# Kernel tuning notes

Hardware: AMD Instinct MI355X
Metric: run time of the kernel (lower is better)

Reference implementation:

```python
import jax, jax.numpy as jnp
import numpy as np

N = 50000   # nodes
E = 800000  # edges
H = 3       # attention heads
IN_F = 128
HID = 128
NUM_CLASSES = 6
GAT_SLOPE = 0.2   # DGL GATConv internal leaky_relu slope
ACT_SLOPE = 0.01  # nn.LeakyReLU default


def setup_inputs() -> dict:
    key = jax.random.key(0)
    ks = jax.random.split(key, 24)
    s = 0.05
    inp = {
        "in_feat": jax.random.normal(ks[0], (N, IN_F), jnp.float32),
        "src": jax.random.randint(ks[1], (E,), 0, N, jnp.int32),
        "dst": jax.random.randint(ks[2], (E,), 0, N, jnp.int32),
        # GATConv 1: W (IN_F, H*HID), attn vectors (H, HID), bias (H*HID)
        "W1": jax.random.normal(ks[3], (IN_F, H * HID), jnp.float32) * s,
        "al1": jax.random.normal(ks[4], (H, HID), jnp.float32) * s,
        "ar1": jax.random.normal(ks[5], (H, HID), jnp.float32) * s,
        "b1": jnp.zeros((H * HID,), jnp.float32),
        # GATConv 2
        "W2": jax.random.normal(ks[6], (HID, H * HID), jnp.float32) * s,
        "al2": jax.random.normal(ks[7], (H, HID), jnp.float32) * s,
        "ar2": jax.random.normal(ks[8], (H, HID), jnp.float32) * s,
        "b2": jnp.zeros((H * HID,), jnp.float32),
    }
    # Dense MLP head lin1..lin4 (HID->HID) and lin5 (HID->NUM_CLASSES)
    for i in range(1, 5):
        inp[f"lw{i}"] = jax.random.normal(ks[8 + 2 * i], (HID, HID), jnp.float32) * s
        inp[f"lb{i}"] = jnp.zeros((HID,), jnp.float32)
    inp["lw5"] = jax.random.normal(ks[20], (HID, NUM_CLASSES), jnp.float32) * s
    inp["lb5"] = jnp.zeros((NUM_CLASSES,), jnp.float32)
    return inp


def gat_conv(x, src, dst, W, al, ar, b):
    # x: (N, F_in) -> out: (N, H, HID)
    h = (x @ W).reshape(N, H, HID)
    el = jnp.einsum('nhf,hf->nh', h, al)  # (N, H)
    er = jnp.einsum('nhf,hf->nh', h, ar)
    e = jax.nn.leaky_relu(el[src] + er[dst], GAT_SLOPE)  # (E, H)
    # edge softmax over incoming edges of each dst node
    m = jax.ops.segment_max(e, dst, num_segments=N)
    m = jnp.where(jnp.isfinite(m), m, 0.0)
    ex = jnp.exp(e - m[dst])
    denom = jax.ops.segment_sum(ex, dst, num_segments=N)
    alpha = ex / (denom[dst] + 1e-9)  # (E, H)
    out = jax.ops.segment_sum(alpha[:, :, None] * h[src], dst, num_segments=N)
    return out + b.reshape(1, H, HID)


def reference(in_feat, src, dst, W1, al1, ar1, b1, W2, al2, ar2, b2,
              lw1, lb1, lw2, lb2, lw3, lb3, lw4, lb4, lw5, lb5):
    act = lambda x: jax.nn.leaky_relu(x, ACT_SLOPE)
    h = act(gat_conv(in_feat, src, dst, W1, al1, ar1, b1)).mean(axis=1)
    h = act(gat_conv(h, src, dst, W2, al2, ar2, b2)).mean(axis=1)
    h = act(h @ lw1 + lb1)
    h = act(h @ lw2 + lb2)
    h = act(h @ lw3 + lb3)
    h = act(h @ lw4 + lb4)
    return h @ lw5 + lb5
```

## Files before the change

### kernel.cpp

```cpp
#include <hip/hip_runtime.h>
#include <hip/hip_bf16.h>


typedef __attribute__((ext_vector_type(8))) short short8;
typedef __attribute__((ext_vector_type(4))) float float4v;

__device__ inline short f2bf(float x) {
    union { float f; unsigned u; } v; v.f = x;
    unsigned r = v.u + 0x7FFFu + ((v.u >> 16) & 1u);
    return (short)(r >> 16);
}
__device__ inline float bf2f(short b) {
    union { float f; unsigned u; } v;
    v.u = ((unsigned)(unsigned short)b) << 16;
    return v.f;
}
__device__ inline short8 zero8() { short8 z = {0,0,0,0,0,0,0,0}; return z; }

__device__ __forceinline__ void gl_lds16(const short* g, short* l) {
    __builtin_amdgcn_global_load_lds(
        (const __attribute__((address_space(1))) void*)g,
        (__attribute__((address_space(3))) void*)l,
        16, 0, 0);
}

#define SW(r) ((((r) >> 2) ^ (r)) & 3)

#define BM 128
#define BN 128
#define BK 32
#define MSTR 136
#define MROWS 64

__global__ void prep_kernel(
    const float* __restrict__ in_feat, short* __restrict__ P1h,
    int n4, int cb, int wb,
    const int* __restrict__ dst, int* __restrict__ cnt, int E,
    const float* __restrict__ w1, const float* __restrict__ w2,
    const float* __restrict__ m1, const float* __restrict__ m2,
    const float* __restrict__ m3, const float* __restrict__ m4,
    const float* __restrict__ w5,
    short* __restrict__ w1h, short* __restrict__ w2h,
    short* __restrict__ m1h, short* __restrict__ m1l,
    short* __restrict__ m2h, short* __restrict__ m2l,
    short* __restrict__ m3h, short* __restrict__ m3l,
    short* __restrict__ m4h, short* __restrict__ m4l,
    short* __restrict__ w5h, short* __restrict__ w5l,
    const float* __restrict__ al1, const float* __restrict__ ar1,
    const float* __restrict__ al2, const float* __restrict__ ar2,
    float* __restrict__ u1, float* __restrict__ u2)
{
    int blk = blockIdx.x;
    if (blk < cb) {
        int i = blk * 256 + threadIdx.x;
        if (i >= n4) return;
        float4 v = *(const float4*)(in_feat + (size_t)i * 4);
        float xs[4] = {v.x, v.y, v.z, v.w};
        short hs[4];
        #pragma unroll
        for (int j = 0; j < 4; ++j) hs[j] = f2bf(xs[j]);
        *(uint2*)(P1h + (size_t)i * 4) = *(uint2*)hs;
    } else if (blk < cb + wb) {
        int j = (blk - cb) * 256 + threadIdx.x;
        const float* src; short* th; short* tl; int Nc, base;
        if      (j < 49152)  { src = w1; th = w1h; tl = nullptr; Nc = 384; base = 0; }
        else if (j < 98304)  { src = w2; th = w2h; tl = nullptr; Nc = 384; base = 49152; }
        else if (j < 114688) { src = m1; th = m1h; tl = m1l; Nc = 128; base = 98304; }
        else if (j < 131072) { src = m2; th = m2h; tl = m2l; Nc = 128; base = 114688; }
        else if (j < 147456) { src = m3; th = m3h; tl = m3l; Nc = 128; base = 131072; }
        else if (j < 163840) { src = m4; th = m4h; tl = m4l; Nc = 128; base = 147456; }
        else if (j < 164608) { src = w5; th = w5h; tl = w5l; Nc = 6;   base = 163840; }
        else return;
        int i = j - base;
        int k = i / Nc, c = i - k * Nc;
        float v = src[i];
        short h = f2bf(v);
        th[(size_t)c * 128 + k] = h;
        if (tl) tl[(size_t)c * 128 + k] = f2bf(v - bf2f(h));
    } else if (blk == cb + wb) {
        int t = threadIdx.x;
        const float* W  = (t < 128) ? w1 : w2;
        const float* av = (t < 128) ? al1 : al2;
        const float* rv = (t < 128) ? ar1 : ar2;
        float* u = (t < 128) ? u1 : u2;
        int k = t & 127;
        #pragma unroll
        for (int h = 0; h < 3; ++h) {
            float sl = 0.f, sr = 0.f;
            for (int f = 0; f < 128; ++f) {
                float wv = W[(size_t)k * 384 + h * 128 + f];
                sl += wv * av[h * 128 + f];
                sr += wv * rv[h * 128 + f];
            }
            u[(h * 2 + 0) * 128 + k] = sl;
            u[(h * 2 + 1) * 128 + k] = sr;
        }
    } else {
        int e = (blk - cb - wb - 1) * 256 + threadIdx.x;
        if (e < E) atomicAdd(&cnt[dst[e]], 1);
    }
}

template <bool BF16>
__global__ __launch_bounds__(256) void node_el(
    const void* __restrict__ Xv, const float* __restrict__ u,
    float* __restrict__ els, float* __restrict__ er, int N)
{
    int n = blockIdx.x * 4 + (threadIdx.x >> 6);
    int l = threadIdx.x & 63;
    if (n >= N) return;
    float x0, x1;
    if (BF16) {
        unsigned v = *(const unsigned*)((const short*)Xv + (size_t)n * 128 + 2 * l);
        union { unsigned u; float f; } f0, f1;
        f0.u = v << 16; f1.u = v & 0xffff0000u;
        x0 = f0.f; x1 = f1.f;
    } else {
        float2 x = *(const float2*)((const float*)Xv + (size_t)n * 128 + 2 * l);
        x0 = x.x; x1 = x.y;
    }
    float a[6];
    #pragma unroll
    for (int v = 0; v < 6; ++v)
        a[v] = x0 * u[v * 128 + 2 * l] + x1 * u[v * 128 + 2 * l + 1];
    #pragma unroll
    for (int msk = 1; msk < 64; msk <<= 1)
        #pragma unroll
        for (int v = 0; v < 6; ++v)
            a[v] += __shfl_xor(a[v], msk);
    if (l == 0) {
        #pragma unroll
        for (int h = 0; h < 3; ++h) {
            els[(size_t)(n * 3 + h) * 2] = a[h * 2];
            er[n * 3 + h] = a[h * 2 + 1];
        }
    }
}

__global__ __launch_bounds__(256) void gemm_mfma(
    const short* __restrict__ Ahi, const short* __restrict__ Bth,
    unsigned char* __restrict__ Cq, float* __restrict__ els,
    int M, int Nc)
{
    __shared__ short Ah[BM * BK], Bh[BN * BK];

    int tid = threadIdx.x, lane = tid & 63, wave = tid >> 6;
    int l15 = lane & 15, q = lane >> 4;
    int rowBase = blockIdx.y * BM, colBase = blockIdx.x * BN;

    float4v acc[2][8];
    #pragma unroll
    for (int mt = 0; mt < 2; ++mt)
        #pragma unroll
        for (int nt = 0; nt < 8; ++nt)
            acc[mt][nt] = (float4v){0.f, 0.f, 0.f, 0.f};

    for (int k0 = 0; k0 < 128; k0 += BK) {
        #pragma unroll
        for (int i = 0; i < 2; ++i) {
            int cid = tid + i * 256;
            int r = cid >> 2, sub = cid & 3;
            int gs = (sub ^ SW(r)) * 8;
            gl_lds16(Ahi + (size_t)(rowBase + r) * 128 + k0 + gs, Ah + cid * 8);
            gl_lds16(Bth + (size_t)(colBase + r) * 128 + k0 + gs, Bh + cid * 8);
        }
        __syncthreads();

        short8 aH[2];
        #pragma unroll
        for (int mt = 0; mt < 2; ++mt) {
            int row = wave * 32 + mt * 16 + l15;
            int off = row * 32 + (q ^ SW(row)) * 8;
            aH[mt] = *(short8*)&Ah[off];
        }
        #pragma unroll
        for (int nt = 0; nt < 8; ++nt) {
            int row = nt * 16 + l15;
            int off = row * 32 + (q ^ SW(row)) * 8;
            short8 bH = *(short8*)&Bh[off];
            #pragma unroll
            for (int mt = 0; mt < 2; ++mt)
                acc[mt][nt] = __builtin_amdgcn_mfma_f32_16x16x32_bf16(aH[mt], bH, acc[mt][nt], 0, 0, 0);
        }
        __syncthreads();
    }

    #pragma unroll
    for (int mt = 0; mt < 2; ++mt) {
        #pragma unroll
        for (int i = 0; i < 4; ++i) {
            float rm = 0.f;
            #pragma unroll
            for (int nt = 0; nt < 8; ++nt)
                rm = fmaxf(rm, fabsf(acc[mt][nt][i]));
            #pragma unroll
            for (int mask = 1; mask < 16; mask <<= 1)
                rm = fmaxf(rm, __shfl_xor(rm, mask));
            int r = rowBase + wave * 32 + mt * 16 + q * 4 + i;
            float inv = 127.f / fmaxf(rm, 1e-30f);
            if (l15 == 0 && r < M)
                els[(size_t)(r * 3 + blockIdx.x) * 2 + 1] = rm * (1.f / 127.f);
            #pragma unroll
            for (int nt = 0; nt < 8; ++nt) {
                int c = colBase + nt * 16 + l15;
                int qi = (int)rintf(acc[mt][nt][i] * inv);
                int qn = __shfl_xor(qi, 1);
                if (!(l15 & 1) && r < M && c < Nc) {
                    unsigned short pk = (unsigned short)((qi & 0xFF) | ((qn & 0xFF) << 8));
                    *(unsigned short*)(Cq + (size_t)r * Nc + c) = pk;
                }
            }
        }
    }
}

__global__ __launch_bounds__(256) void mlp_fused(
    const short* __restrict__ Ph, const short* __restrict__ Pl,
    const short* __restrict__ w1h, const short* __restrict__ w1l,
    const short* __restrict__ w2h, const short* __restrict__ w2l,
    const short* __restrict__ w3h, const short* __restrict__ w3l,
    const short* __restrict__ w4h, const short* __restrict__ w4l,
    const short* __restrict__ w5h, const short* __restrict__ w5l,
    const float* __restrict__ b1, const float* __restrict__ b2,
    const float* __restrict__ b3, const float* __restrict__ b4,
    const float* __restrict__ b5,
    float* __restrict__ out, int M)
{
    __shared__ short AH[MROWS * MSTR], AL[MROWS * MSTR];
    __shared__ short WH[128 * BK], WL[128 * BK];

    int tid = threadIdx.x, lane = tid & 63, wave = tid >> 6;
    int l15 = lane & 15, q = lane >> 4;
    int rowBase = blockIdx.x * MROWS;

    #pragma unroll
    for (int s = 0; s < 4; ++s) {
        int idx = tid + s * 256;
        int r = idx >> 4, kq = (idx & 15) * 8;
        int gr = rowBase + r;
        short8 vh = zero8(), vl = zero8();
        if (gr < M) {
            vh = *(const short8*)(Ph + (size_t)gr * 128 + kq);
            vl = *(const short8*)(Pl + (size_t)gr * 128 + kq);
        }
        *(short8*)&AH[r * MSTR + kq] = vh;
        *(short8*)&AL[r * MSTR + kq] = vl;
    }

    const short* Whs[4] = {w1h, w2h, w3h, w4h};
    const short* Wls[4] = {w1l, w2l, w3l, w4l};
    const float* Bss[4] = {b1, b2, b3, b4};

    #pragma unroll
    for (int L = 0; L < 4; ++L) {
        float4v acc[8];
        #pragma unroll
        for (int nt = 0; nt < 8; ++nt)
            acc[nt] = (float4v){0.f, 0.f, 0.f, 0.f};

        for (int k0 = 0; k0 < 128; k0 += BK) {
            #pragma unroll
            for (int i = 0; i < 4; ++i) {
                int c2 = tid + (i & 1) * 256;
                int r = c2 >> 2, sub = c2 & 3;
                int gs = (sub ^ SW(r)) * 8;
                if (i < 2) gl_lds16(Whs[L] + (size_t)r * 128 + k0 + gs, WH + c2 * 8);
                else       gl_lds16(Wls[L] + (size_t)r * 128 + k0 + gs, WL + c2 * 8);
            }
            __syncthreads();
            int offa = (wave * 16 + l15) * MSTR + k0 + q * 8;
            short8 aH  = *(short8*)&AH[offa];
            short8 aL2 = *(short8*)&AL[offa];
            #pragma unroll
            for (int nt = 0; nt < 8; ++nt) {
                int row = nt * 16 + l15;
                int off = row * 32 + (q ^ SW(row)) * 8;
                short8 bH = *(short8*)&WH[off];
                short8 bL = *(short8*)&WL[off];
                acc[nt] = __builtin_amdgcn_mfma_f32_16x16x32_bf16(aH, bH, acc[nt], 0, 0, 0);
                acc[nt] = __builtin_amdgcn_mfma_f32_16x16x32_bf16(aH, bL, acc[nt], 0, 0, 0);
                acc[nt] = __builtin_amdgcn_mfma_f32_16x16x32_bf16(aL2, bH, acc[nt], 0, 0, 0);
            }
            __syncthreads();
        }
        #pragma unroll
        for (int nt = 0; nt < 8; ++nt) {
            int c = nt * 16 + l15;
            float bv = Bss[L][c];
            #pragma unroll
            for (int i = 0; i < 4; ++i) {
                int r = wave * 16 + q * 4 + i;
                float v = acc[nt][i] + bv;
                v = (v < 0.f) ? 0.01f * v : v;
                short hh = f2bf(v);
                AH[r * MSTR + c] = hh;
                AL[r * MSTR + c] = f2bf(v - bf2f(hh));
            }
        }
        __syncthreads();
    }

    float4v acc5 = (float4v){0.f, 0.f, 0.f, 0.f};
    for (int k0 = 0; k0 < 128; k0 += BK) {
        if (tid < 128) {
            int plane = tid >> 6, rem = tid & 63;
            int c = rem >> 2, sub = rem & 3;
            short8 v = zero8();
            if (c < 6)
                v = *(const short8*)((plane ? w5l : w5h) + (size_t)c * 128 + k0 + sub * 8);
            *(short8*)&((plane ? WL : WH)[c * 32 + (sub ^ SW(c)) * 8]) = v;
        }
        __syncthreads();
        int offa = (wave * 16 + l15) * MSTR + k0 + q * 8;
        short8 aH  = *(short8*)&AH[offa];
        short8 aL2 = *(short8*)&AL[offa];
        int offb = l15 * 32 + (q ^ SW(l15)) * 8;
        short8 bH = *(short8*)&WH[offb];
        short8 bL = *(short8*)&WL[offb];
        acc5 = __builtin_amdgcn_mfma_f32_16x16x32_bf16(aH, bH, acc5, 0, 0, 0);
        acc5 = __builtin_amdgcn_mfma_f32_16x16x32_bf16(aH, bL, acc5, 0, 0, 0);
        acc5 = __builtin_amdgcn_mfma_f32_16x16x32_bf16(aL2, bH, acc5, 0, 0, 0);
        __syncthreads();
    }
    if (l15 < 6) {
        float bv = b5[l15];
        #pragma unroll
        for (int i = 0; i < 4; ++i) {
            int r = rowBase + wave * 16 + q * 4 + i;
            if (r < M) out[(size_t)r * 6 + l15] = acc5[i] + bv;
        }
    }
}

__global__ __launch_bounds__(1024) void scan_block(const int* __restrict__ cnt,
                                                   int* __restrict__ off,
                                                   int* __restrict__ bsum, int n)
{
    __shared__ int tmp[1024];
    int tid = threadIdx.x;
    int i = blockIdx.x * 1024 + tid;
    int v = (i < n) ? cnt[i] : 0;
    tmp[tid] = v;
    __syncthreads();
    for (int s = 1; s < 1024; s <<= 1) {
        int t = (tid >= s) ? tmp[tid - s] : 0;
        __syncthreads();
        tmp[tid] += t;
        __syncthreads();
    }
    if (i < n) off[i] = tmp[tid] - v;
    if (tid == 1023) bsum[blockIdx.x] = tmp[1023];
}

__global__ void scan_add2(int* __restrict__ off, const int* __restrict__ bsum,
                          int n, int nb)
{
    __shared__ int pre[64];
    int tid = threadIdx.x;
    if (tid < 64) {
        int v = (tid < nb) ? bsum[tid] : 0;
        #pragma unroll
        for (int s = 1; s < 64; s <<= 1) {
            int t = __shfl_up(v, s);
            if (tid >= s) v += t;
        }
        pre[tid] = v;
    }
    __syncthreads();
    int i = blockIdx.x * blockDim.x + tid;
    if (i < n) {
        int chunk = i >> 10;
        off[i] += chunk ? pre[chunk - 1] : 0;
    }
    if (i == 0) off[n] = pre[nb - 1];
}

__global__ void scatter_kernel(const int* __restrict__ src, const int* __restrict__ dst,
                               const int* __restrict__ off, int* __restrict__ cnt,
                               int* __restrict__ csrc, int E)
{
    int e = blockIdx.x * blockDim.x + threadIdx.x;
    if (e < E) {
        int d = dst[e];
        int p = atomicSub(&cnt[d], 1) - 1;
        csrc[off[d] + p] = src[e];
    }
}

__global__ __launch_bounds__(384) void agg_kernel(
    const unsigned char* __restrict__ h8, const float* __restrict__ els,
    const float* __restrict__ er, const int* __restrict__ off,
    const int* __restrict__ csrc, const float* __restrict__ bias,
    short* __restrict__ outH, short* __restrict__ outL, int N)
{
    int tid = threadIdx.x;
    int u = tid >> 6;
    int nl = u / 3;
    int head = u - nl * 3;
    int l = tid & 63;
    int n = blockIdx.x * 2 + nl;
    bool active = (n < N);

    __shared__ int   ssrcS[6][64];
    __shared__ float swS[6][64];
    __shared__ float smS[2][384];

    int beg = 0, deg = 0;
    float erv = 0.f;
    if (active) {
        beg = off[n];
        deg = off[n + 1] - beg;
        erv = er[n * 3 + head];
    }

    const unsigned char* hseg = h8 + head * 128 + l * 2;
    float ax = 0.f, ay = 0.f, denl = 0.f;

    for (int base = 0; base < deg; base += 64) {
        int cnt = min(64, deg - base);
        int s_l = 0; float w = 0.f, wS = 0.f;
        if (l < cnt) {
            s_l = csrc[beg + base + l];
            float2 e2 = *(const float2*)(els + (size_t)(s_l * 3 + head) * 2);
            float t = e2.x + erv;
            t = (t < 0.f) ? 0.2f * t : t;
            w = __expf(t);
            wS = w * e2.y;
        }
        denl += w;
        ssrcS[u][l] = s_l;
        swS[u][l]   = wS;
        for (int q0 = 0; q0 < cnt; q0 += 8) {
            int sA[8]; float wA[8]; unsigned vA[8];
            #pragma unroll
            for (int b = 0; b < 8; ++b) {
                int e = q0 + b;
                sA[b] = ssrcS[u][e];
                wA[b] = swS[u][e];
            }
            #pragma unroll
            for (int b = 0; b < 8; ++b)
                vA[b] = *(const unsigned short*)(hseg + (size_t)sA[b] * 384);
            #pragma unroll
            for (int b = 0; b < 8; ++b) {
                int b0 = (int)(signed char)(vA[b] & 0xFF);
                int b1 = (int)(signed char)((vA[b] >> 8) & 0xFF);
                ax += wA[b] * (float)b0;
                ay += wA[b] * (float)b1;
            }
        }
    }

    float den = denl;
    #pragma unroll
    for (int msk = 1; msk < 64; msk <<= 1) den += __shfl_xor(den, msk);
    float r = 1.f / (den + 1e-9f);
    if (deg == 0) r = 0.f;

    if (active) {
        int fb = head * 128 + 2 * l;
        float2 bv = *(const float2*)(bias + fb);
        float vx = ax * r + bv.x; vx = (vx < 0.f) ? 0.01f * vx : vx;
        float vy = ay * r + bv.y; vy = (vy < 0.f) ? 0.01f * vy : vy;
        smS[nl][fb]     = vx;
        smS[nl][fb + 1] = vy;
    }
    __syncthreads();
    if (tid < 128) {
        int mn = tid >> 6;
        int n2 = blockIdx.x * 2 + mn;
        if (n2 < N) {
            int f0i = (tid & 63) * 2, f1i = f0i + 1;
            float mx = (smS[mn][f0i] + smS[mn][128 + f0i] + smS[mn][256 + f0i]) * (1.0f / 3.0f);
            float my = (smS[mn][f1i] + smS[mn][128 + f1i] + smS[mn][256 + f1i]) * (1.0f / 3.0f);
            short hx = f2bf(mx), hy = f2bf(my);
            unsigned ph = (unsigned)(unsigned short)hx | ((unsigned)(unsigned short)hy << 16);
            *(unsigned*)(outH + (size_t)n2 * 128 + f0i) = ph;
            if (outL) {
                short lx = f2bf(mx - bf2f(hx)), ly = f2bf(my - bf2f(hy));
                unsigned pl = (unsigned)(unsigned short)lx | ((unsigned)(unsigned short)ly << 16);
                *(unsigned*)(outL + (size_t)n2 * 128 + f0i) = pl;
            }
        }
    }
}

extern "C" void kernel_launch(void* const* d_in, const int* in_sizes, int n_in,
                              void* d_out, int out_size, void* d_ws, size_t ws_size,
                              hipStream_t stream)
{
    const float* in_feat = (const float*)d_in[0];
    const int*   src     = (const int*)d_in[1];
    const int*   dst     = (const int*)d_in[2];
    const float* W1  = (const float*)d_in[3];
    const float* al1 = (const float*)d_in[4];
    const float* ar1 = (const float*)d_in[5];
    const float* b1  = (const float*)d_in[6];
    const float* W2  = (const float*)d_in[7];
    const float* al2 = (const float*)d_in[8];
    const float* ar2 = (const float*)d_in[9];
    const float* b2  = (const float*)d_in[10];
    const float* lw1 = (const float*)d_in[11];
    const float* lb1 = (const float*)d_in[12];
    const float* lw2 = (const float*)d_in[13];
    const float* lb2 = (const float*)d_in[14];
    const float* lw3 = (const float*)d_in[15];
    const float* lb3 = (const float*)d_in[16];
    const float* lw4 = (const float*)d_in[17];
    const float* lb4 = (const float*)d_in[18];
    const float* lw5 = (const float*)d_in[19];
    const float* lb5 = (const float*)d_in[20];

    const int N = in_sizes[0] / 128;
    const int E = in_sizes[1];

    size_t o = 0;
    auto alloc = [&](size_t bytes) { size_t p = o; o = (o + bytes + 255) & ~(size_t)255; return p; };
    char* ws = (char*)d_ws;
    short* P1h = (short*)(ws + alloc((size_t)N * 128 * 2));
    short* P1l = (short*)(ws + alloc((size_t)N * 128 * 2));
    short* P2h = (short*)(ws + alloc((size_t)N * 128 * 2));
    unsigned char* Aq = (unsigned char*)(ws + alloc((size_t)N * 384));
    float* els1 = (float*)(ws + alloc((size_t)N * 3 * 2 * 4));
    float* er1  = (float*)(ws + alloc((size_t)N * 3 * 4));
    float* els2 = (float*)(ws + alloc((size_t)N * 3 * 2 * 4));
    float* er2  = (float*)(ws + alloc((size_t)N * 3 * 4));
    float* u1   = (float*)(ws + alloc((size_t)6 * 128 * 4));
    float* u2   = (float*)(ws + alloc((size_t)6 * 128 * 4));
    int*   cnt  = (int*)(ws + alloc((size_t)N * 4));
    int*   off  = (int*)(ws + alloc((size_t)(N + 1) * 4));
    int*   bsum = (int*)(ws + alloc((size_t)4096));
    int*   csrc = (int*)(ws + alloc((size_t)E * 4));
    short* w1th = (short*)(ws + alloc((size_t)384 * 128 * 2));
    short* w2th = (short*)(ws + alloc((size_t)384 * 128 * 2));
    short* l1th = (short*)(ws + alloc((size_t)128 * 128 * 2));
    short* l1tl = (short*)(ws + alloc((size_t)128 * 128 * 2));
    short* l2th = (short*)(ws + alloc((size_t)128 * 128 * 2));
    short* l2tl = (short*)(ws + alloc((size_t)128 * 128 * 2));
    short* l3th = (short*)(ws + alloc((size_t)128 * 128 * 2));
    short* l3tl = (short*)(ws + alloc((size_t)128 * 128 * 2));
    short* l4th = (short*)(ws + alloc((size_t)128 * 128 * 2));
    short* l4tl = (short*)(ws + alloc((size_t)128 * 128 * 2));
    short* l5th = (short*)(ws + alloc((size_t)6 * 128 * 2));
    short* l5tl = (short*)(ws + alloc((size_t)6 * 128 * 2));
    (void)ws_size;

    float* out = (float*)d_out;

    hipMemsetAsync(cnt, 0, (size_t)N * 4, stream);
    int n4 = N * 128 / 4;
    int cb = (n4 + 255) / 256;
    int wb = (164608 + 255) / 256;
    int hb = (E + 255) / 256;
    prep_kernel<<<cb + wb + 1 + hb, 256, 0, stream>>>(
        in_feat, P1h, n4, cb, wb, dst, cnt, E,
        W1, W2, lw1, lw2, lw3, lw4, lw5,
        w1th, w2th, l1th, l1tl, l2th, l2tl,
        l3th, l3tl, l4th, l4tl, l5th, l5tl,
        al1, ar1, al2, ar2, u1, u2);

    int nb = (N + 1023) / 1024;
    scan_block<<<nb, 1024, 0, stream>>>(cnt, off, bsum, N);
    scan_add2<<<(N + 255) / 256, 256, 0, stream>>>(off, bsum, N, nb);
    scatter_kernel<<<(E + 255) / 256, 256, 0, stream>>>(src, dst, off, cnt, csrc, E);
    node_el<false><<<(N + 3) / 4, 256, 0, stream>>>(in_feat, u1, els1, er1, N);

    int RB = (N + BM - 1) / BM;
    dim3 ggrid(3, RB);
    int AGB = (N + 1) / 2;

    gemm_mfma<<<ggrid, 256, 0, stream>>>(P1h, w1th, Aq, els1, N, 384);
    agg_kernel<<<AGB, 384, 0, stream>>>(Aq, els1, er1, off, csrc, b1,
                                        P2h, nullptr, N);

    node_el<true><<<(N + 3) / 4, 256, 0, stream>>>(P2h, u2, els2, er2, N);

    gemm_mfma<<<ggrid, 256, 0, stream>>>(P2h, w2th, Aq, els2, N, 384);
    agg_kernel<<<AGB, 384, 0, stream>>>(Aq, els2, er2, off, csrc, b2,
                                        P1h, P1l, N);

    int RBM = (N + MROWS - 1) / MROWS;
    mlp_fused<<<RBM, 256, 0, stream>>>(P1h, P1l,
                                       l1th, l1tl, l2th, l2tl, l3th, l3tl,
                                       l4th, l4tl, l5th, l5tl,
                                       lb1, lb2, lb3, lb4, lb5, out, N);
}
```

Before: 508.8 us.

## Merge layer-1 GEMM, CSR scatter and attention logits into one launch; fuse logits into layer-2 GEMM

Layer-1 GEMM, the CSR edge scatter and the node attention-logit computation are independent, so they now run as one heterogeneous launch with block ranges dispatched by index. Scatter and logit blocks use grid-stride loops. In layer 2, the el/er dot products are computed inside the GEMM from the bf16 A tiles already staged in LDS, which removes the separate node_el pass and its reread of the features. The aim is fewer launches, better overlap of small kernels, and less memory traffic, at the cost of extra per-lane FMAs and LDS reads inside the GEMM loop.

```diff
diff --git a/kernel.cpp b/kernel.cpp
--- a/kernel.cpp
+++ b/kernel.cpp
@@ -101,52 +101,24 @@
     }
 }
 
-template <bool BF16>
-__global__ __launch_bounds__(256) void node_el(
-    const void* __restrict__ Xv, const float* __restrict__ u,
-    float* __restrict__ els, float* __restrict__ er, int N)
-{
-    int n = blockIdx.x * 4 + (threadIdx.x >> 6);
-    int l = threadIdx.x & 63;
-    if (n >= N) return;
-    float x0, x1;
-    if (BF16) {
-        unsigned v = *(const unsigned*)((const short*)Xv + (size_t)n * 128 + 2 * l);
-        union { unsigned u; float f; } f0, f1;
-        f0.u = v << 16; f1.u = v & 0xffff0000u;
-        x0 = f0.f; x1 = f1.f;
-    } else {
-        float2 x = *(const float2*)((const float*)Xv + (size_t)n * 128 + 2 * l);
-        x0 = x.x; x1 = x.y;
-    }
-    float a[6];
-    #pragma unroll
-    for (int v = 0; v < 6; ++v)
-        a[v] = x0 * u[v * 128 + 2 * l] + x1 * u[v * 128 + 2 * l + 1];
-    #pragma unroll
-    for (int msk = 1; msk < 64; msk <<= 1)
-        #pragma unroll
-        for (int v = 0; v < 6; ++v)
-            a[v] += __shfl_xor(a[v], msk);
-    if (l == 0) {
-        #pragma unroll
-        for (int h = 0; h < 3; ++h) {
-            els[(size_t)(n * 3 + h) * 2] = a[h * 2];
-            er[n * 3 + h] = a[h * 2 + 1];
-        }
-    }
-}
-
-__global__ __launch_bounds__(256) void gemm_mfma(
+template <bool LOG>
+__device__ __forceinline__ void gemm_body(
     const short* __restrict__ Ahi, const short* __restrict__ Bth,
     unsigned char* __restrict__ Cq, float* __restrict__ els,
-    int M, int Nc)
+    float* __restrict__ erv, const float* __restrict__ uvec,
+    int M, int Nc, int head, int rby)
 {
     __shared__ short Ah[BM * BK], Bh[BN * BK];
+    __shared__ float uL[2][128];
 
     int tid = threadIdx.x, lane = tid & 63, wave = tid >> 6;
     int l15 = lane & 15, q = lane >> 4;
-    int rowBase = blockIdx.y * BM, colBase = blockIdx.x * BN;
+    int rowBase = rby * BM, colBase = head * BN;
+
+    if (LOG) {
+        int s = tid >> 7, k = tid & 127;
+        uL[s][k] = uvec[(head * 2 + s) * 128 + k];
+    }
 
     float4v acc[2][8];
     #pragma unroll
@@ -154,6 +126,7 @@
         #pragma unroll
         for (int nt = 0; nt < 8; ++nt)
             acc[mt][nt] = (float4v){0.f, 0.f, 0.f, 0.f};
+    float pl[2] = {0.f, 0.f}, pr[2] = {0.f, 0.f};
 
     for (int k0 = 0; k0 < 128; k0 += BK) {
         #pragma unroll
@@ -173,6 +146,17 @@
             int off = row * 32 + (q ^ SW(row)) * 8;
             aH[mt] = *(short8*)&Ah[off];
         }
+        if (LOG) {
+            #pragma unroll
+            for (int mt = 0; mt < 2; ++mt)
+                #pragma unroll
+                for (int j = 0; j < 8; ++j) {
+                    float av = bf2f(aH[mt][j]);
+                    int k = k0 + q * 8 + j;
+                    pl[mt] += av * uL[0][k];
+                    pr[mt] += av * uL[1][k];
+                }
+        }
         #pragma unroll
         for (int nt = 0; nt < 8; ++nt) {
             int row = nt * 16 + l15;
@@ -183,6 +167,21 @@
                 acc[mt][nt] = __builtin_amdgcn_mfma_f32_16x16x32_bf16(aH[mt], bH, acc[mt][nt], 0, 0, 0);
         }
         __syncthreads();
+    }
+
+    if (LOG) {
+        #pragma unroll
+        for (int mt = 0; mt < 2; ++mt) {
+            pl[mt] += __shfl_xor(pl[mt], 16);
+            pl[mt] += __shfl_xor(pl[mt], 32);
+            pr[mt] += __shfl_xor(pr[mt], 16);
+            pr[mt] += __shfl_xor(pr[mt], 32);
+            int r = rowBase + wave * 32 + mt * 16 + l15;
+            if (q == 0 && r < M) {
+                els[(size_t)(r * 3 + head) * 2] = pl[mt];
+                erv[r * 3 + head] = pr[mt];
+            }
+        }
     }
 
     #pragma unroll
@@ -199,10 +198,10 @@
             int r = rowBase + wave * 32 + mt * 16 + q * 4 + i;
             float inv = 127.f / fmaxf(rm, 1e-30f);
             if (l15 == 0 && r < M)
-                els[(size_t)(r * 3 + blockIdx.x) * 2 + 1] = rm * (1.f / 127.f);
+                els[(size_t)(r * 3 + head) * 2 + 1] = rm * (1.f / 127.f);
             #pragma unroll
             for (int nt = 0; nt < 8; ++nt) {
-                int c = colBase + nt * 16 + l15;
+                int c = head * BN + nt * 16 + l15;
                 int qi = (int)rintf(acc[mt][nt][i] * inv);
                 int qn = __shfl_xor(qi, 1);
                 if (!(l15 & 1) && r < M && c < Nc) {
@@ -212,6 +211,63 @@
             }
         }
     }
+}
+
+__global__ __launch_bounds__(256) void l1_mega(
+    const short* __restrict__ P1h, const short* __restrict__ w1th,
+    unsigned char* __restrict__ Cq, float* __restrict__ els1, int M, int Nc,
+    int NG,
+    const int* __restrict__ src, const int* __restrict__ dst,
+    const int* __restrict__ off, int* __restrict__ cnt,
+    int* __restrict__ csrc, int E, int NS,
+    const float* __restrict__ X, const float* __restrict__ u1,
+    float* __restrict__ er1, int N, int NE)
+{
+    int b = blockIdx.x;
+    if (b < NG) {
+        gemm_body<false>(P1h, w1th, Cq, els1, nullptr, nullptr,
+                         M, Nc, b % 3, b / 3);
+        return;
+    }
+    b -= NG;
+    if (b < NS) {
+        for (int e = b * 256 + threadIdx.x; e < E; e += NS * 256) {
+            int d = dst[e];
+            int p = atomicSub(&cnt[d], 1) - 1;
+            csrc[off[d] + p] = src[e];
+        }
+        return;
+    }
+    b -= NS;
+    int wv = threadIdx.x >> 6, l = threadIdx.x & 63;
+    for (int n = b * 4 + wv; n < N; n += NE * 4) {
+        float2 x = *(const float2*)(X + (size_t)n * 128 + 2 * l);
+        float a[6];
+        #pragma unroll
+        for (int v = 0; v < 6; ++v)
+            a[v] = x.x * u1[v * 128 + 2 * l] + x.y * u1[v * 128 + 2 * l + 1];
+        #pragma unroll
+        for (int msk = 1; msk < 64; msk <<= 1)
+            #pragma unroll
+            for (int v = 0; v < 6; ++v)
+                a[v] += __shfl_xor(a[v], msk);
+        if (l == 0) {
+            #pragma unroll
+            for (int h = 0; h < 3; ++h) {
+                els1[(size_t)(n * 3 + h) * 2] = a[h * 2];
+                er1[n * 3 + h] = a[h * 2 + 1];
+            }
+        }
+    }
+}
+
+__global__ __launch_bounds__(256) void gemm_l2(
+    const short* __restrict__ P2h, const short* __restrict__ w2th,
+    unsigned char* __restrict__ Cq, float* __restrict__ els2,
+    float* __restrict__ er2, const float* __restrict__ u2, int M, int Nc)
+{
+    gemm_body<true>(P2h, w2th, Cq, els2, er2, u2, M, Nc,
+                    blockIdx.x, blockIdx.y);
 }
 
 __global__ __launch_bounds__(256) void mlp_fused(
@@ -373,18 +429,6 @@
         off[i] += chunk ? pre[chunk - 1] : 0;
     }
     if (i == 0) off[n] = pre[nb - 1];
-}
-
-__global__ void scatter_kernel(const int* __restrict__ src, const int* __restrict__ dst,
-                               const int* __restrict__ off, int* __restrict__ cnt,
-                               int* __restrict__ csrc, int E)
-{
-    int e = blockIdx.x * blockDim.x + threadIdx.x;
-    if (e < E) {
-        int d = dst[e];
-        int p = atomicSub(&cnt[d], 1) - 1;
-        csrc[off[d] + p] = src[e];
-    }
 }
 
 __global__ __launch_bounds__(384) void agg_kernel(
@@ -562,20 +606,21 @@
     int nb = (N + 1023) / 1024;
     scan_block<<<nb, 1024, 0, stream>>>(cnt, off, bsum, N);
     scan_add2<<<(N + 255) / 256, 256, 0, stream>>>(off, bsum, N, nb);
-    scatter_kernel<<<(E + 255) / 256, 256, 0, stream>>>(src, dst, off, cnt, csrc, E);
-    node_el<false><<<(N + 3) / 4, 256, 0, stream>>>(in_feat, u1, els1, er1, N);
 
     int RB = (N + BM - 1) / BM;
-    dim3 ggrid(3, RB);
+    int NG = 3 * RB, NS = 512, NE = 1024;
     int AGB = (N + 1) / 2;
 
-    gemm_mfma<<<ggrid, 256, 0, stream>>>(P1h, w1th, Aq, els1, N, 384);
+    l1_mega<<<NG + NS + NE, 256, 0, stream>>>(
+        P1h, w1th, Aq, els1, N, 384, NG,
+        src, dst, off, cnt, csrc, E, NS,
+        in_feat, u1, er1, N, NE);
+
     agg_kernel<<<AGB, 384, 0, stream>>>(Aq, els1, er1, off, csrc, b1,
                                         P2h, nullptr, N);
 
-    node_el<true><<<(N + 3) / 4, 256, 0, stream>>>(P2h, u2, els2, er2, N);
-
-    gemm_mfma<<<ggrid, 256, 0, stream>>>(P2h, w2th, Aq, els2, N, 384);
+    gemm_l2<<<dim3(3, RB), 256, 0, stream>>>(P2h, w2th, Aq, els2, er2, u2,
+                                             N, 384);
     agg_kernel<<<AGB, 384, 0, stream>>>(Aq, els2, er2, off, csrc, b2,
                                         P1h, P1l, N);
 
```

Measured after the change: 500.1 us. No clear change (-1.7%).
